# Optimization experiments

Measured on AMD Instinct MI355X. Metric: run time of the kernel, lower is better.

Reference implementation:

```python
import jax, jax.numpy as jnp
import numpy as np

NODE_SIZE = 100000
DIM = 512
B = 2048
GAMMA = 3.0
LAMB = 20.0
TAU = 8.0


def setup_inputs() -> dict:
    key = jax.random.key(0)
    k1, k2 = jax.random.split(key)
    pairs = jax.random.randint(k1, (B, 2), 0, NODE_SIZE, dtype=jnp.int64 if jax.config.jax_enable_x64 else jnp.int32)
    emb = jax.random.normal(k2, (NODE_SIZE, DIM), dtype=jnp.float32)
    return {"pairs": pairs, "emb": emb}


def _align_loss(pairs, emb):
    l = pairs[:, 0]
    r = pairs[:, 1]
    l_emb = emb[l]                     # [B, D]
    r_emb = emb[r]                     # [B, D]
    pos_dis = jnp.sum(jnp.square(l_emb - r_emb), axis=-1, keepdims=True)  # [B, 1]

    emb_sq = jnp.sum(jnp.square(emb), axis=1)          # [N]

    def squared_dist(A):
        # ||a||^2 + ||b||^2 - 2 a.b  -> [B, N]
        a_sq = jnp.sum(jnp.square(A), axis=1, keepdims=True)
        return a_sq + emb_sq[None, :] - 2.0 * (A @ emb.T)

    l_neg_dis = squared_dist(l_emb)
    r_neg_dis = squared_dist(r_emb)

    # mask = 1 - one_hot(l) - one_hot(r), built without materializing one-hots
    rows = jnp.arange(B)
    mask = jnp.ones((B, NODE_SIZE), dtype=emb.dtype)
    mask = mask.at[rows, l].add(-1.0)
    mask = mask.at[rows, r].add(-1.0)

    def norm_lse(loss):
        loss = loss * mask
        mu = jax.lax.stop_gradient(jnp.mean(loss, axis=-1, keepdims=True))
        sd = jax.lax.stop_gradient(jnp.std(loss, axis=-1, keepdims=True))  # unbiased=False
        loss = (loss - mu) / sd
        return jax.scipy.special.logsumexp(LAMB * loss + TAU, axis=-1)

    l_loss = norm_lse(pos_dis - l_neg_dis + GAMMA)
    r_loss = norm_lse(pos_dis - r_neg_dis + GAMMA)
    return jnp.mean(l_loss + r_loss)


def reference(pairs, emb):
    return _align_loss(pairs, emb)
```

## Files before the change

kernel.cpp:

```cpp
#include <hip/hip_runtime.h>
#include <stdint.h>

#define NODES   100000
#define NPAD    100096
#define DIM     512
#define NPAIR   2048
#define MROWS   4096
#define NB      782
#define MPAGES  32
#define GAMMA_F 3.0f
#define LAMB_F  20.0f
#define TAU_F   8.0f
#define SHIFT_F 140.0f

#define TM 128
#define TN 128
#define BK 64

typedef __attribute__((ext_vector_type(8))) short          short8;
typedef __attribute__((ext_vector_type(8))) unsigned short ushort8;
typedef __attribute__((ext_vector_type(4))) float          f32x4;


__device__ __forceinline__ unsigned short f2bf(float f) {
    unsigned u = __float_as_uint(f);
    u += 0x7FFFu + ((u >> 16) & 1u);
    return (unsigned short)(u >> 16);
}
__device__ __forceinline__ float bf2f(unsigned short h) {
    return __uint_as_float(((unsigned)h) << 16);
}

__device__ __forceinline__ void gload_lds16(const void* g, void* l) {
    unsigned lofs = (unsigned)__builtin_amdgcn_readfirstlane((unsigned)(uintptr_t)l);
    auto lp = reinterpret_cast<__attribute__((address_space(3))) unsigned*>(lofs);
    auto gp = (const __attribute__((address_space(1))) unsigned*)g;
    __builtin_amdgcn_global_load_lds(gp, lp, 16, 0, 0);
}


__global__ void convert_stats_kernel(const float* __restrict__ emb,
                                     unsigned short* __restrict__ Ebf,
                                     float* __restrict__ esq,
                                     float* __restrict__ Spart,
                                     float* __restrict__ Tpart,
                                     float* __restrict__ E1part,
                                     float* __restrict__ E2part) {
    __shared__ float Sl[4][512];
    __shared__ float Tl[4][512];
    __shared__ float ew[8];
    const int b = blockIdx.x, t = threadIdx.x;
    const int lane = t & 63, wave = t >> 6;
    const int r0 = b * 196;
    float sacc[8], tacc[8];
    #pragma unroll
    for (int k = 0; k < 8; ++k) { sacc[k] = 0.f; tacc[k] = 0.f; }
    float e1 = 0.f, e2 = 0.f;
    for (int i = 0; i < 49; ++i) {
        const int row = r0 + i * 4 + wave;
        if (row >= NPAD) continue;
        const bool real = row < NODES;
        float v[8];
        float ss = 0.f;
        if (real) {
            const float4* p = (const float4*)(emb + (size_t)row * DIM + lane * 8);
            float4 a = p[0], bb = p[1];
            v[0]=a.x; v[1]=a.y; v[2]=a.z; v[3]=a.w;
            v[4]=bb.x; v[5]=bb.y; v[6]=bb.z; v[7]=bb.w;
            #pragma unroll
            for (int k = 0; k < 8; ++k) ss += v[k] * v[k];
        } else {
            #pragma unroll
            for (int k = 0; k < 8; ++k) v[k] = 0.f;
        }
        #pragma unroll
        for (int o = 1; o < 64; o <<= 1) ss += __shfl_xor(ss, o);
        ushort8 o8;
        float vr[8];
        #pragma unroll
        for (int k = 0; k < 8; ++k) { o8[k] = f2bf(v[k]); vr[k] = bf2f(o8[k]); }
        *(ushort8*)(Ebf + (size_t)row * DIM + lane * 8) = o8;
        if (lane == 0) esq[row] = ss;
        if (real) {
            #pragma unroll
            for (int k = 0; k < 8; ++k) { sacc[k] += vr[k]; tacc[k] += ss * vr[k]; }
            if (lane == 0) { e1 += ss; e2 += ss * ss; }
        }
    }
    #pragma unroll
    for (int k = 0; k < 8; ++k) {
        Sl[wave][lane * 8 + k] = sacc[k];
        Tl[wave][lane * 8 + k] = tacc[k];
    }
    if (lane == 0) { ew[wave] = e1; ew[4 + wave] = e2; }
    __syncthreads();
    #pragma unroll
    for (int kk = 0; kk < 2; ++kk) {
        const int d = 2 * t + kk;
        Spart[(size_t)b * 512 + d] = Sl[0][d] + Sl[1][d] + Sl[2][d] + Sl[3][d];
        Tpart[(size_t)b * 512 + d] = Tl[0][d] + Tl[1][d] + Tl[2][d] + Tl[3][d];
    }
    if (t == 0) E1part[b] = ew[0] + ew[1] + ew[2] + ew[3];
    if (t == 1) E2part[b] = ew[4] + ew[5] + ew[6] + ew[7];
}

__global__ void stats_merge_kernel(const float* __restrict__ Spart,
                                   const float* __restrict__ Tpart,
                                   const float* __restrict__ E1part,
                                   const float* __restrict__ E2part,
                                   float* __restrict__ Svec,
                                   float* __restrict__ Tvec,
                                   double* __restrict__ E12) {
    const int bid = blockIdx.x, t = threadIdx.x;
    if (bid < 32) {
        __shared__ float part[8][32];
        const int col = (bid & 15) * 32 + (t & 31);
        const int seg = t >> 5;
        const float* src = (bid < 16) ? Spart : Tpart;
        float s = 0.f;
        const int b0 = seg * 64;
        for (int b = b0; b < b0 + 64; ++b) s += src[(size_t)b * 512 + col];
        part[seg][t & 31] = s;
        __syncthreads();
        if (t < 32) {
            float r = 0.f;
            #pragma unroll
            for (int g = 0; g < 8; ++g) r += part[g][t];
            const int c2 = (bid & 15) * 32 + t;
            if (bid < 16) Svec[c2] = r; else Tvec[c2] = r;
        }
    } else {
        __shared__ double w[4];
        const float* src = (bid == 32) ? E1part : E2part;
        double s = (double)src[t] + (double)src[t + 256];
        #pragma unroll
        for (int o = 1; o < 64; o <<= 1) s += __shfl_xor(s, o);
        if ((t & 63) == 0) w[t >> 6] = s;
        __syncthreads();
        if (t == 0) E12[bid - 32] = w[0] + w[1] + w[2] + w[3];
    }
}

__global__ void gather_kernel(const int* __restrict__ pairs,
                              const float* __restrict__ emb,
                              unsigned short* __restrict__ Abf,
                              float* __restrict__ cvec,
                              float* __restrict__ posv) {
    const int p    = blockIdx.x;
    const int lane = threadIdx.x;
    const int li = pairs[2 * p], ri = pairs[2 * p + 1];
    const float4* pl = (const float4*)(emb + (size_t)li * DIM + lane * 8);
    const float4* pr = (const float4*)(emb + (size_t)ri * DIM + lane * 8);
    float4 a0 = pl[0], a1 = pl[1];
    float4 b0 = pr[0], b1 = pr[1];
    float la[8] = {a0.x,a0.y,a0.z,a0.w,a1.x,a1.y,a1.z,a1.w};
    float lb[8] = {b0.x,b0.y,b0.z,b0.w,b1.x,b1.y,b1.z,b1.w};
    float sa = 0.f, sb = 0.f, sd = 0.f;
    ushort8 oa, ob;
    #pragma unroll
    for (int i = 0; i < 8; ++i) {
        sa += la[i] * la[i];
        sb += lb[i] * lb[i];
        float d = la[i] - lb[i];
        sd += d * d;
        oa[i] = f2bf(la[i]);
        ob[i] = f2bf(lb[i]);
    }
    *(ushort8*)(Abf + (size_t)p * DIM + lane * 8)            = oa;
    *(ushort8*)(Abf + (size_t)(NPAIR + p) * DIM + lane * 8)  = ob;
    #pragma unroll
    for (int off = 1; off < 64; off <<= 1) {
        sa += __shfl_xor(sa, off);
        sb += __shfl_xor(sb, off);
        sd += __shfl_xor(sd, off);
    }
    if (lane == 0) {
        cvec[p]         = sd - sa + GAMMA_F;
        cvec[NPAIR + p] = sd - sb + GAMMA_F;
        posv[p]         = sd;
    }
}


#define GPAD 520

__launch_bounds__(256, 2)
__global__ void gram_kernel(const unsigned short* __restrict__ Ebf,
                            float* __restrict__ Gpart) {
    __shared__ unsigned short ldsA[16 * GPAD];
    __shared__ unsigned short ldsB[16 * GPAD];
    const int tid  = threadIdx.x;
    const int lane = tid & 63;
    const int wave = tid >> 6;
    const int wx = wave & 1, wy = wave >> 1;
    const int d1base = blockIdx.y * 128;
    const int d2base = blockIdx.x * 128;
    const int bz = blockIdx.z;
    const int r15 = lane & 15, q = lane >> 4;

    f32x4 zero4 = {0.f, 0.f, 0.f, 0.f};
    f32x4 acc[4][4];
    #pragma unroll
    for (int i = 0; i < 4; ++i)
        #pragma unroll
        for (int j = 0; j < 4; ++j) acc[i][j] = zero4;

    for (int jc = bz; jc < NPAD / 64; jc += 32) {
        const int j0 = jc * 64;
        #pragma unroll
        for (int ii = 0; ii < 4; ++ii) {
            const int iss = wave * 4 + ii;
            const int row = iss * 4 + (lane >> 4);
            gload_lds16(Ebf + (size_t)(j0 + row) * DIM + d1base + (lane & 15) * 8,
                        &ldsA[iss * GPAD]);
            gload_lds16(Ebf + (size_t)(j0 + row) * DIM + d2base + (lane & 15) * 8,
                        &ldsB[iss * GPAD]);
        }
        __builtin_amdgcn_s_waitcnt(0);
        __syncthreads();
        #pragma unroll
        for (int h = 0; h < 2; ++h) {
            short8 af[4], bfv[4];
            #pragma unroll
            for (int mt = 0; mt < 4; ++mt) {
                const int m = wy * 64 + mt * 16 + r15;
                #pragma unroll
                for (int i = 0; i < 8; ++i) {
                    const int r = h * 32 + q * 8 + i;
                    af[mt][i] = (short)ldsA[(r >> 2) * GPAD + (r & 3) * 128 + m];
                }
            }
            #pragma unroll
            for (int nt = 0; nt < 4; ++nt) {
                const int n = wx * 64 + nt * 16 + r15;
                #pragma unroll
                for (int i = 0; i < 8; ++i) {
                    const int r = h * 32 + q * 8 + i;
                    bfv[nt][i] = (short)ldsB[(r >> 2) * GPAD + (r & 3) * 128 + n];
                }
            }
            #pragma unroll
            for (int mt = 0; mt < 4; ++mt)
                #pragma unroll
                for (int nt = 0; nt < 4; ++nt)
                    acc[mt][nt] = __builtin_amdgcn_mfma_f32_16x16x32_bf16(
                        af[mt], bfv[nt], acc[mt][nt], 0, 0, 0);
        }
        __syncthreads();
    }
    float* gp = Gpart + (size_t)bz * 512 * 512;
    #pragma unroll
    for (int mt = 0; mt < 4; ++mt)
        #pragma unroll
        for (int r = 0; r < 4; ++r) {
            const int d1 = d1base + wy * 64 + mt * 16 + q * 4 + r;
            #pragma unroll
            for (int nt = 0; nt < 4; ++nt) {
                const int d2 = d2base + wx * 64 + nt * 16 + r15;
                gp[d1 * 512 + d2] = acc[mt][nt][r];
            }
        }
}

__global__ void gram_merge_kernel(const float* __restrict__ Gpart,
                                  float* __restrict__ G) {
    const int idx = blockIdx.x * 256 + threadIdx.x;
    float s = 0.f;
    for (int b = 0; b < 32; ++b) s += Gpart[(size_t)b * 512 * 512 + idx];
    G[idx] = s;
}


__launch_bounds__(256)
__global__ void gu_kernel(const unsigned short* __restrict__ Abf,
                          const float* __restrict__ G,
                          const float* __restrict__ Svec,
                          const float* __restrict__ Tvec,
                          const double* __restrict__ E12,
                          const float* __restrict__ cvec,
                          const float* __restrict__ posv,
                          const int* __restrict__ pairs,
                          float* __restrict__ alpha_v,
                          float* __restrict__ shift_v) {
    __shared__ float u[8][512];
    __shared__ float red[8][3][4];
    const int t = threadIdx.x;
    const int lane = t & 63, wave = t >> 6;
    const int r0 = blockIdx.x * 8;
    #pragma unroll
    for (int p = 0; p < 8; ++p) {
        unsigned pk = *(const unsigned*)(Abf + (size_t)(r0 + p) * DIM + 2 * t);
        u[p][2 * t]     = bf2f((unsigned short)(pk & 0xffffu));
        u[p][2 * t + 1] = bf2f((unsigned short)(pk >> 16));
    }
    __syncthreads();
    float acc0[8], acc1[8];
    #pragma unroll
    for (int p = 0; p < 8; ++p) { acc0[p] = 0.f; acc1[p] = 0.f; }
    for (int d1 = 0; d1 < 512; ++d1) {
        const float2 g = *(const float2*)(G + d1 * 512 + 2 * t);
        #pragma unroll
        for (int p = 0; p < 8; ++p) {
            const float up = u[p][d1];
            acc0[p] += up * g.x;
            acc1[p] += up * g.y;
        }
    }
    const float sv0 = Svec[2 * t], sv1 = Svec[2 * t + 1];
    const float tv0 = Tvec[2 * t], tv1 = Tvec[2 * t + 1];
    #pragma unroll
    for (int p = 0; p < 8; ++p) {
        const float u0 = u[p][2 * t], u1 = u[p][2 * t + 1];
        float pdS = u0 * sv0 + u1 * sv1;
        float pdT = u0 * tv0 + u1 * tv1;
        float pq  = u0 * acc0[p] + u1 * acc1[p];
        #pragma unroll
        for (int off = 1; off < 64; off <<= 1) {
            pdS += __shfl_xor(pdS, off);
            pdT += __shfl_xor(pdT, off);
            pq  += __shfl_xor(pq,  off);
        }
        if (lane == 0) {
            red[p][0][wave] = pdS;
            red[p][1][wave] = pdT;
            red[p][2][wave] = pq;
        }
    }
    __syncthreads();
    if (t < 8) {
        const int p = t;
        const double dS = (double)red[p][0][0] + red[p][0][1] + red[p][0][2] + red[p][0][3];
        const double dT = (double)red[p][1][0] + red[p][1][1] + red[p][1][2] + red[p][1][3];
        const double qq = (double)red[p][2][0] + red[p][2][1] + red[p][2][2] + red[p][2][3];
        const int row = r0 + p;
        const int pp  = row & (NPAIR - 1);
        const double c  = (double)cvec[row];
        const double E1 = E12[0], E2 = E12[1];
        const double N  = (double)NODES;
        double Sx  = N * c + 2.0 * dS - E1;
        double Sxx = (N * c * c - 2.0 * c * E1 + E2) + 4.0 * (c * dS - dT) + 4.0 * qq;
        const int li = pairs[2 * pp], ri = pairs[2 * pp + 1];
        const double pos = (double)posv[pp];
        if (li != ri) {
            const double x1 = pos + (double)GAMMA_F, x2 = (double)GAMMA_F;
            Sx  -= x1 + x2;
            Sxx -= x1 * x1 + x2 * x2;
        } else {
            Sx -= 2.0 * (double)GAMMA_F;
        }
        const double mu  = Sx / N;
        const double var = Sxx / N - mu * mu;
        const double sd  = sqrt(fmax(var, 1e-30));
        const double al  = (double)LAMB_F / sd;
        alpha_v[row] = (float)al;
        shift_v[row] = (float)(al * mu + (double)SHIFT_F);
    }
}


__launch_bounds__(256, 2)
__global__ void gemm_kernel(const unsigned short* __restrict__ Abf,
                            const unsigned short* __restrict__ Ebf,
                            const float* __restrict__ cvec,
                            const float* __restrict__ esq,
                            const int*   __restrict__ pairs,
                            const float* __restrict__ alpha_v,
                            const float* __restrict__ shift_v,
                            float* __restrict__ psum) {
    __shared__ unsigned short ldsA[TM * BK];
    __shared__ unsigned short ldsB[TN * BK];
    __shared__ float red_s[2][TM];
    __shared__ float alsh[TM], csh[TM], cmsh[TM];
    __shared__ int   lish[TM], rish[TM];

    const int tid  = threadIdx.x;
    const int lane = tid & 63;
    const int wave = tid >> 6;
    const int wx = wave & 1;
    const int wy = wave >> 1;
    const int nb = blockIdx.x;
    const int n0 = nb * TN;
    const int m0 = blockIdx.y * TM;

    if (tid < TM) {
        const int gm = m0 + tid;
        alsh[tid] = alpha_v[gm];
        csh[tid]  = shift_v[gm];
        cmsh[tid] = cvec[gm];
        const int p = gm & (NPAIR - 1);
        lish[tid] = pairs[2 * p];
        rish[tid] = pairs[2 * p + 1];
    }

    f32x4 zero4 = {0.f, 0.f, 0.f, 0.f};
    f32x4 acc[4][4];
    #pragma unroll
    for (int i = 0; i < 4; ++i)
        #pragma unroll
        for (int j = 0; j < 4; ++j) acc[i][j] = zero4;

    const int lrow   = lane >> 3;
    const int lchunk = lane & 7;
    const int r15 = lane & 15;
    const int q   = lane >> 4;

    for (int kt = 0; kt < DIM / BK; ++kt) {
        const int kb = kt * BK;
        #pragma unroll
        for (int j = 0; j < 4; ++j) {
            const int rbase = (wave * 4 + j) * 8;
            const int row   = rbase + lrow;
            const int gch   = lchunk ^ (row & 7);
            gload_lds16(Abf + ((size_t)(m0 + row) * DIM + kb + gch * 8), &ldsA[rbase * BK]);
            gload_lds16(Ebf + ((size_t)(n0 + row) * DIM + kb + gch * 8), &ldsB[rbase * BK]);
        }
        __builtin_amdgcn_s_waitcnt(0);
        __syncthreads();
        #pragma unroll
        for (int h = 0; h < 2; ++h) {
            short8 af[4], bfr[4];
            #pragma unroll
            for (int mt = 0; mt < 4; ++mt) {
                int row = wy * 64 + mt * 16 + r15;
                int c   = (h * 4 + q) ^ (row & 7);
                af[mt] = *(const short8*)&ldsA[row * BK + c * 8];
            }
            #pragma unroll
            for (int nt = 0; nt < 4; ++nt) {
                int row = wx * 64 + nt * 16 + r15;
                int c   = (h * 4 + q) ^ (row & 7);
                bfr[nt] = *(const short8*)&ldsB[row * BK + c * 8];
            }
            #pragma unroll
            for (int mt = 0; mt < 4; ++mt)
                #pragma unroll
                for (int nt = 0; nt < 4; ++nt)
                    acc[mt][nt] = __builtin_amdgcn_mfma_f32_16x16x32_bf16(
                        af[mt], bfr[nt], acc[mt][nt], 0, 0, 0);
        }
        __syncthreads();
    }

    #pragma unroll
    for (int mt = 0; mt < 4; ++mt) {
        #pragma unroll
        for (int r = 0; r < 4; ++r) {
            const int rit = wy * 64 + mt * 16 + q * 4 + r;
            const float cm = cmsh[rit];
            const float al = alsh[rit];
            const float Cc = csh[rit];
            const int li = lish[rit], ri = rish[rit];
            float se = 0.f;
            #pragma unroll
            for (int nt = 0; nt < 4; ++nt) {
                const int gn = n0 + wx * 64 + nt * 16 + r15;
                float xv = cm + 2.0f * acc[mt][nt][r] - esq[gn];
                float msk = 1.0f - (float)(gn == li) - (float)(gn == ri);
                xv *= msk;
                float term = __expf(fmaf(al, xv, -Cc));
                se += (gn < NODES) ? term : 0.f;
            }
            #pragma unroll
            for (int o = 1; o < 16; o <<= 1) se += __shfl_xor(se, o);
            if (r15 == 0) red_s[wx][rit] = se;
        }
    }
    __syncthreads();
    if (tid < TM) {
        psum[(size_t)nb * MROWS + m0 + tid] = red_s[0][tid] + red_s[1][tid];
    }
}


__global__ void lse_loss_kernel(const float* __restrict__ psum,
                                float* __restrict__ loss_v) {
    const int row = blockIdx.x * 256 + threadIdx.x;
    float s = 0.f;
    for (int nb = 0; nb < NB; ++nb)
        s += psum[(size_t)nb * MROWS + row];
    loss_v[row] = (TAU_F + SHIFT_F) + logf(s);
}

__global__ void final_kernel(const float* __restrict__ loss_v,
                             float* __restrict__ out) {
    __shared__ double wpart[4];
    int t = threadIdx.x;
    double s = 0.0;
    for (int i = t; i < MROWS; i += 256)
        s += (double)loss_v[i];
    #pragma unroll
    for (int off = 1; off < 64; off <<= 1) s += __shfl_xor(s, off);
    if ((t & 63) == 0) wpart[t >> 6] = s;
    __syncthreads();
    if (t == 0) out[0] = (float)((wpart[0] + wpart[1] + wpart[2] + wpart[3]) / (double)NPAIR);
}


extern "C" void kernel_launch(void* const* d_in, const int* in_sizes, int n_in,
                              void* d_out, int out_size, void* d_ws, size_t ws_size,
                              hipStream_t stream) {
    const int*   pairs = (const int*)d_in[0];
    const float* emb   = (const float*)d_in[1];
    float* out = (float*)d_out;

    char* ws = (char*)d_ws;
    size_t off = 0;
    auto alloc = [&](size_t bytes) -> void* {
        void* p = ws + off;
        off += (bytes + 255) & ~(size_t)255;
        return p;
    };
    unsigned short* Ebf = (unsigned short*)alloc((size_t)NPAD * DIM * 2);
    unsigned short* Abf = (unsigned short*)alloc((size_t)MROWS * DIM * 2);
    float*  esq     = (float*)alloc((size_t)NPAD * 4);
    float*  cvec    = (float*)alloc((size_t)MROWS * 4);
    float*  posv    = (float*)alloc((size_t)NPAIR * 4);
    float*  Spart   = (float*)alloc((size_t)512 * DIM * 4);
    float*  Tpart   = (float*)alloc((size_t)512 * DIM * 4);
    float*  E1part  = (float*)alloc((size_t)512 * 4);
    float*  E2part  = (float*)alloc((size_t)512 * 4);
    float*  Svec    = (float*)alloc((size_t)DIM * 4);
    float*  Tvec    = (float*)alloc((size_t)DIM * 4);
    double* E12     = (double*)alloc(2 * sizeof(double));
    float*  G       = (float*)alloc((size_t)512 * 512 * 4);
    float*  alpha_v = (float*)alloc((size_t)MROWS * 4);
    float*  shift_v = (float*)alloc((size_t)MROWS * 4);
    float*  loss_v  = (float*)alloc((size_t)MROWS * 4);
    char* uni = (char*)alloc((size_t)32 * 512 * 512 * 4);
    float* Gpart = (float*)uni;
    float* psum  = (float*)uni;
    if (off > ws_size) return;

    convert_stats_kernel<<<512, 256, 0, stream>>>(emb, Ebf, esq,
                                                  Spart, Tpart, E1part, E2part);
    stats_merge_kernel<<<34, 256, 0, stream>>>(Spart, Tpart, E1part, E2part,
                                               Svec, Tvec, E12);
    gather_kernel<<<NPAIR, 64, 0, stream>>>(pairs, emb, Abf, cvec, posv);

    gram_kernel<<<dim3(4, 4, 32), 256, 0, stream>>>(Ebf, Gpart);
    gram_merge_kernel<<<1024, 256, 0, stream>>>(Gpart, G);
    gu_kernel<<<MROWS / 8, 256, 0, stream>>>(Abf, G, Svec, Tvec, E12,
                                             cvec, posv, pairs, alpha_v, shift_v);

    gemm_kernel<<<dim3(NB, MPAGES), 256, 0, stream>>>(Abf, Ebf, cvec, esq, pairs,
                                                      alpha_v, shift_v, psum);
    lse_loss_kernel<<<16, 256, 0, stream>>>(psum, loss_v);
    final_kernel<<<1, 256, 0, stream>>>(loss_v, out);
}
```

Baseline: 979.0 us.

## Compute only upper-triangular Gram tiles and split LSE row reduction across blocks

The Gram matrix kernel now computes only the 10 upper-triangular 128x128 tile pairs of the symmetric 512x512 product instead of all 16, and raises the split along the node axis from 32 to 48 slices so more blocks run. The merge kernel reads the mirrored tile with transposed offsets to rebuild the full matrix. The final per-row reduction over 782 partial sums is split into 4 chunks across more blocks, followed by a small combine kernel, which adds one extra launch.

```diff
diff --git a/kernel.cpp b/kernel.cpp
--- a/kernel.cpp
+++ b/kernel.cpp
@@ -16,6 +16,7 @@
 #define TM 128
 #define TN 128
 #define BK 64
+#define GZ 48
 
 typedef __attribute__((ext_vector_type(8))) short          short8;
 typedef __attribute__((ext_vector_type(8))) unsigned short ushort8;
@@ -193,9 +194,12 @@
     const int lane = tid & 63;
     const int wave = tid >> 6;
     const int wx = wave & 1, wy = wave >> 1;
-    const int d1base = blockIdx.y * 128;
-    const int d2base = blockIdx.x * 128;
-    const int bz = blockIdx.z;
+    const int pr  = blockIdx.x;
+    const int by  = (pr >= 4) + (pr >= 7) + (pr >= 9);
+    const int bx  = pr - (by * (7 - by)) / 2;
+    const int d1base = by * 128;
+    const int d2base = bx * 128;
+    const int bz = blockIdx.y;
     const int r15 = lane & 15, q = lane >> 4;
 
     f32x4 zero4 = {0.f, 0.f, 0.f, 0.f};
@@ -205,7 +209,7 @@
         #pragma unroll
         for (int j = 0; j < 4; ++j) acc[i][j] = zero4;
 
-    for (int jc = bz; jc < NPAD / 64; jc += 32) {
+    for (int jc = bz; jc < NPAD / 64; jc += GZ) {
         const int j0 = jc * 64;
         #pragma unroll
         for (int ii = 0; ii < 4; ++ii) {
@@ -248,16 +252,16 @@
         }
         __syncthreads();
     }
-    float* gp = Gpart + (size_t)bz * 512 * 512;
+    float* gp = Gpart + ((size_t)bz * 10 + pr) * (128 * 128);
     #pragma unroll
     for (int mt = 0; mt < 4; ++mt)
         #pragma unroll
         for (int r = 0; r < 4; ++r) {
-            const int d1 = d1base + wy * 64 + mt * 16 + q * 4 + r;
+            const int l1 = wy * 64 + mt * 16 + q * 4 + r;
             #pragma unroll
             for (int nt = 0; nt < 4; ++nt) {
-                const int d2 = d2base + wx * 64 + nt * 16 + r15;
-                gp[d1 * 512 + d2] = acc[mt][nt][r];
+                const int l2 = wx * 64 + nt * 16 + r15;
+                gp[l1 * 128 + l2] = acc[mt][nt][r];
             }
         }
 }
@@ -265,8 +269,15 @@
 __global__ void gram_merge_kernel(const float* __restrict__ Gpart,
                                   float* __restrict__ G) {
     const int idx = blockIdx.x * 256 + threadIdx.x;
+    const int d1 = idx >> 9, d2 = idx & 511;
+    const int bi = d1 >> 7, bj = d2 >> 7;
+    const int r1 = d1 & 127, r2 = d2 & 127;
+    int p, off;
+    if (bi <= bj) { p = (bi * (7 - bi)) / 2 + bj; off = r1 * 128 + r2; }
+    else          { p = (bj * (7 - bj)) / 2 + bi; off = r2 * 128 + r1; }
     float s = 0.f;
-    for (int b = 0; b < 32; ++b) s += Gpart[(size_t)b * 512 * 512 + idx];
+    for (int bz = 0; bz < GZ; ++bz)
+        s += Gpart[((size_t)bz * 10 + p) * (128 * 128) + off];
     G[idx] = s;
 }
 
@@ -472,12 +483,23 @@
 }
 
 
-__global__ void lse_loss_kernel(const float* __restrict__ psum,
-                                float* __restrict__ loss_v) {
+__global__ void lse_part_kernel(const float* __restrict__ psum,
+                                float* __restrict__ lsep) {
     const int row = blockIdx.x * 256 + threadIdx.x;
+    const int c   = blockIdx.y;
+    const int nb0 = c * 196;
+    const int nb1 = (nb0 + 196 < NB) ? nb0 + 196 : NB;
     float s = 0.f;
-    for (int nb = 0; nb < NB; ++nb)
+    for (int nb = nb0; nb < nb1; ++nb)
         s += psum[(size_t)nb * MROWS + row];
+    lsep[(size_t)c * MROWS + row] = s;
+}
+
+__global__ void loss_kernel(const float* __restrict__ lsep,
+                            float* __restrict__ loss_v) {
+    const int row = blockIdx.x * 256 + threadIdx.x;
+    const float s = lsep[row] + lsep[MROWS + row]
+                  + lsep[2 * MROWS + row] + lsep[3 * MROWS + row];
     loss_v[row] = (TAU_F + SHIFT_F) + logf(s);
 }
 
@@ -525,6 +547,7 @@
     float*  G       = (float*)alloc((size_t)512 * 512 * 4);
     float*  alpha_v = (float*)alloc((size_t)MROWS * 4);
     float*  shift_v = (float*)alloc((size_t)MROWS * 4);
+    float*  lsep    = (float*)alloc((size_t)4 * MROWS * 4);
     float*  loss_v  = (float*)alloc((size_t)MROWS * 4);
     char* uni = (char*)alloc((size_t)32 * 512 * 512 * 4);
     float* Gpart = (float*)uni;
@@ -537,13 +560,14 @@
                                                Svec, Tvec, E12);
     gather_kernel<<<NPAIR, 64, 0, stream>>>(pairs, emb, Abf, cvec, posv);
 
-    gram_kernel<<<dim3(4, 4, 32), 256, 0, stream>>>(Ebf, Gpart);
+    gram_kernel<<<dim3(10, GZ), 256, 0, stream>>>(Ebf, Gpart);
     gram_merge_kernel<<<1024, 256, 0, stream>>>(Gpart, G);
     gu_kernel<<<MROWS / 8, 256, 0, stream>>>(Abf, G, Svec, Tvec, E12,
                                              cvec, posv, pairs, alpha_v, shift_v);
 
     gemm_kernel<<<dim3(NB, MPAGES), 256, 0, stream>>>(Abf, Ebf, cvec, esq, pairs,
                                                       alpha_v, shift_v, psum);
-    lse_loss_kernel<<<16, 256, 0, stream>>>(psum, loss_v);
+    lse_part_kernel<<<dim3(16, 4), 256, 0, stream>>>(psum, lsep);
+    loss_kernel<<<16, 256, 0, stream>>>(lsep, loss_v);
     final_kernel<<<1, 256, 0, stream>>>(loss_v, out);
 }
```

After: 1.055 ms. +7.8%, slower.
